# Optimization experiments

Measured on AMD Instinct MI355X. Metric: run time of the kernel, lower is better.

Reference implementation:

```python
import jax, jax.numpy as jnp
import numpy as np

C_IN = 256   # in_channels
D = 256      # hidden_dim
RNN_OUT = 2 * D  # bidir concat
K = 80       # num_classes - 1
B, H, W = 16, 64, 64


def setup_inputs() -> dict:
    key = jax.random.key(0)
    ks = jax.random.split(key, 32)
    sD = 1.0 / np.sqrt(D)
    sR = 1.0 / np.sqrt(RNN_OUT)
    f32 = jnp.float32
    inp = {}
    inp["feat"] = jax.random.normal(ks[0], (B, C_IN, H, W), f32)
    # 1x1 conv projection (acts as per-pixel linear)
    inp["proj_w"] = jax.random.normal(ks[1], (D, C_IN), f32) * sD
    inp["proj_b"] = jnp.zeros((D,), f32)
    # FastRNN forward-direction cell
    inp["Wf"] = jax.random.normal(ks[2], (D, D), f32) * sD
    inp["Uf"] = jax.random.normal(ks[3], (D, D), f32) * sD
    inp["bf"] = jnp.zeros((D,), f32)
    inp["alpha_f"] = jnp.asarray(-3.0, f32)  # sigmoid(-3) ~ 0.05 (FastRNN init)
    inp["beta_f"] = jnp.asarray(3.0, f32)    # sigmoid(3)  ~ 0.95
    # FastRNN backward-direction cell
    inp["Wb"] = jax.random.normal(ks[4], (D, D), f32) * sD
    inp["Ub"] = jax.random.normal(ks[5], (D, D), f32) * sD
    inp["bb"] = jnp.zeros((D,), f32)
    inp["alpha_b"] = jnp.asarray(-3.0, f32)
    inp["beta_b"] = jnp.asarray(3.0, f32)
    # cls MLP: Linear(RNN_OUT,RNN_OUT) -> ReLU -> Linear(RNN_OUT,K)
    inp["cls_w1"] = jax.random.normal(ks[6], (RNN_OUT, RNN_OUT), f32) * sR
    inp["cls_b1"] = jnp.zeros((RNN_OUT,), f32)
    inp["cls_w2"] = jax.random.normal(ks[7], (K, RNN_OUT), f32) * sR
    inp["cls_b2"] = jnp.zeros((K,), f32)
    # reg MLP -> 4
    inp["reg_w1"] = jax.random.normal(ks[8], (RNN_OUT, RNN_OUT), f32) * sR
    inp["reg_b1"] = jnp.zeros((RNN_OUT,), f32)
    inp["reg_w2"] = jax.random.normal(ks[9], (4, RNN_OUT), f32) * sR
    inp["reg_b2"] = jnp.zeros((4,), f32)
    # ctr MLP -> 1
    inp["ctr_w1"] = jax.random.normal(ks[10], (RNN_OUT, RNN_OUT), f32) * sR
    inp["ctr_b1"] = jnp.zeros((RNN_OUT,), f32)
    inp["ctr_w2"] = jax.random.normal(ks[11], (1, RNN_OUT), f32) * sR
    inp["ctr_b2"] = jnp.zeros((1,), f32)
    return inp


def _fastrnn_scan(pre, U, alpha, beta):
    # pre: (S, B, D) = W x_t + b precomputed for all steps
    a = jax.nn.sigmoid(alpha)
    b = jax.nn.sigmoid(beta)
    def step(h, p):
        h_new = a * jnp.tanh(p + h @ U.T) + b * h
        return h_new, h_new
    h0 = jnp.zeros(pre.shape[1:], pre.dtype)
    _, hs = jax.lax.scan(step, h0, pre)
    return hs  # (S, B, D)


def _mlp(h, w1, b1, w2, b2):
    return jax.nn.relu(h @ w1.T + b1) @ w2.T + b2


def reference(feat, proj_w, proj_b, Wf, Uf, bf, alpha_f, beta_f,
              Wb, Ub, bb, alpha_b, beta_b,
              cls_w1, cls_b1, cls_w2, cls_b2,
              reg_w1, reg_b1, reg_w2, reg_b2,
              ctr_w1, ctr_b1, ctr_w2, ctr_b2):
    Bn, C, Hn, Wn = feat.shape
    # 1x1 conv proj then flatten spatial tokens: (B, S, D)
    x = jnp.einsum('bchw,dc->bhwd', feat, proj_w) + proj_b
    x = x.reshape(Bn, Hn * Wn, D)
    # forward-direction FastRNN
    pre_f = (x @ Wf.T + bf).transpose(1, 0, 2)           # (S, B, D)
    h_f = _fastrnn_scan(pre_f, Uf, alpha_f, beta_f).transpose(1, 0, 2)
    # backward-direction FastRNN
    pre_b = (x[:, ::-1] @ Wb.T + bb).transpose(1, 0, 2)
    h_b = _fastrnn_scan(pre_b, Ub, alpha_b, beta_b).transpose(1, 0, 2)[:, ::-1]
    h = jnp.concatenate([h_f, h_b], axis=-1)             # (B, S, 2D)
    cls = _mlp(h, cls_w1, cls_b1, cls_w2, cls_b2)
    reg = _mlp(h, reg_w1, reg_b1, reg_w2, reg_b2)
    ctr = _mlp(h, ctr_w1, ctr_b1, ctr_w2, ctr_b2)
    cls = cls.reshape(Bn, Hn, Wn, K).transpose(0, 3, 1, 2)
    reg = jax.nn.relu(reg.reshape(Bn, Hn, Wn, 4).transpose(0, 3, 1, 2))
    ctr = ctr.reshape(Bn, Hn, Wn, 1).transpose(0, 3, 1, 2)
    return (cls, reg, ctr)
```

## Files before the change

kernel.cpp:

```cpp
#include <hip/hip_runtime.h>
#include <hip/hip_bf16.h>

typedef short bf16x8 __attribute__((ext_vector_type(8)));
typedef float f32x4 __attribute__((ext_vector_type(4)));

__device__ __forceinline__ ushort f2b(float x) {
    __hip_bfloat16 h = __float2bfloat16(x);
    return *reinterpret_cast<ushort*>(&h);
}

__device__ __forceinline__ void gload_lds16(const void* g, void* l) {
    __builtin_amdgcn_global_load_lds(
        (const __attribute__((address_space(1))) void*)g,
        (__attribute__((address_space(3))) void*)l, 16, 0, 0);
}

__global__ __launch_bounds__(256) void prep_mcat(
    const float* __restrict__ proj_w, const float* __restrict__ proj_b,
    const float* __restrict__ Wf, const float* __restrict__ bf_,
    const float* __restrict__ Wb, const float* __restrict__ bb_,
    __hip_bfloat16* __restrict__ Mcat, float* __restrict__ cvec)
{
    int n = blockIdx.x;
    int c = threadIdx.x;
    const float* W    = (n < 256) ? (Wf + n * 256) : (Wb + (n - 256) * 256);
    const float* bias = (n < 256) ? bf_ : bb_;
    float acc = 0.f;
    for (int k = 0; k < 256; ++k)
        acc = fmaf(W[k], proj_w[k * 256 + c], acc);
    Mcat[n * 256 + c] = __float2bfloat16(acc);

    __shared__ float red[256];
    red[c] = W[c] * proj_b[c];
    __syncthreads();
    for (int s = 128; s > 0; s >>= 1) {
        if (c < s) red[c] += red[c + s];
        __syncthreads();
    }
    if (c == 0) cvec[n] = red[0] + bias[n & 255];
}

__global__ __launch_bounds__(256) void prep_weights(
    const float* __restrict__ cls_w1, const float* __restrict__ cls_b1,
    const float* __restrict__ cls_w2, const float* __restrict__ cls_b2,
    const float* __restrict__ reg_w1, const float* __restrict__ reg_b1,
    const float* __restrict__ reg_w2, const float* __restrict__ reg_b2,
    const float* __restrict__ ctr_w1, const float* __restrict__ ctr_b1,
    const float* __restrict__ ctr_w2, const float* __restrict__ ctr_b2,
    __hip_bfloat16* __restrict__ W1cat, float* __restrict__ b1cat,
    __hip_bfloat16* __restrict__ W2pad, float* __restrict__ b2cat)
{
    int idx = blockIdx.x * 256 + threadIdx.x;
    if (idx < 786432) {
        int n = idx >> 9, k = idx & 511;
        const float* src = (n < 512) ? cls_w1 : (n < 1024 ? reg_w1 : ctr_w1);
        int nn = n & 511;
        W1cat[idx] = __float2bfloat16(src[nn * 512 + k]);
    }
    if (idx < 196608) {
        int j = idx / 1536, k = idx % 1536;
        float v = 0.f;
        if (j < 80 && k < 512)                         v = cls_w2[j * 512 + k];
        else if (j >= 80 && j < 84 && k >= 512 && k < 1024) v = reg_w2[(j - 80) * 512 + (k - 512)];
        else if (j == 84 && k >= 1024)                 v = ctr_w2[k - 1024];
        W2pad[idx] = __float2bfloat16(v);
    }
    if (idx < 1536)
        b1cat[idx] = (idx < 512) ? cls_b1[idx] : (idx < 1024 ? reg_b1[idx - 512] : ctr_b1[idx - 1024]);
    if (idx < 96)
        b2cat[idx] = (idx < 80) ? cls_b2[idx] : (idx < 84 ? reg_b2[idx - 80] : (idx == 84 ? ctr_b2[0] : 0.f));
}

__global__ __launch_bounds__(256) void transpose_feat(
    const float* __restrict__ feat, __hip_bfloat16* __restrict__ fx)
{
    __shared__ float tile[32][65];
    int st = blockIdx.x * 64, ct = blockIdx.y * 32, b = blockIdx.z;
    int tid = threadIdx.x;
    int sl = tid & 63, cl = tid >> 6;
    const float* fp = feat + ((size_t)b * 256 + ct) * 4096 + st;
#pragma unroll
    for (int i = 0; i < 8; ++i)
        tile[cl + i * 4][sl] = fp[(size_t)(cl + i * 4) * 4096 + sl];
    __syncthreads();
    int cw = tid & 31, sw = tid >> 5;
#pragma unroll
    for (int i = 0; i < 8; ++i) {
        int ss = st + sw + i * 8;
        fx[((size_t)ss * 16 + b) * 256 + ct + cw] = __float2bfloat16(tile[cw][sw + i * 8]);
    }
}

template <int MODE>
__global__ __launch_bounds__(256) void gemm_bf16(
    const __hip_bfloat16* __restrict__ A, const __hip_bfloat16* __restrict__ B,
    void* __restrict__ Cv, const float* __restrict__ bias, int M, int N, int K)
{
    __shared__ __align__(16) ushort As[128][64];
    __shared__ __align__(16) ushort Bs[128][64];
    const int tid = threadIdx.x;
    const int wv = tid >> 6;
    const int lane = tid & 63;
    const int wm = wv >> 1, wn = wv & 1;
    const int l15 = lane & 15, l4 = lane >> 4;
    const int m0 = blockIdx.y * 128;
    const int n0 = blockIdx.x * 128;

    f32x4 acc[4][4];
#pragma unroll
    for (int i = 0; i < 4; ++i)
#pragma unroll
        for (int j = 0; j < 4; ++j) acc[i][j] = (f32x4){0.f, 0.f, 0.f, 0.f};

    const int c0 = wv * 4 * 64 + lane;
    const ushort* Abase = (const ushort*)A;
    const ushort* Bbase = (const ushort*)B;

    for (int k0 = 0; k0 < K; k0 += 64) {
#pragma unroll
        for (int i = 0; i < 4; ++i) {
            int c = c0 + i * 64;
            int row = c >> 3, kc = c & 7;
            int kcs = (kc ^ (row & 7)) * 8;
            gload_lds16(Abase + (size_t)(m0 + row) * K + k0 + kcs,
                        &As[0][0] + (wv * 4 + i) * 512);
            gload_lds16(Bbase + (size_t)(n0 + row) * K + k0 + kcs,
                        &Bs[0][0] + (wv * 4 + i) * 512);
        }
        asm volatile("s_waitcnt vmcnt(0)" ::: "memory");
        __syncthreads();

#pragma unroll
        for (int ks = 0; ks < 2; ++ks) {
            const int swz = ((ks * 4 + l4) ^ (l15 & 7)) * 8;
            bf16x8 af[4], bf[4];
#pragma unroll
            for (int mi = 0; mi < 4; ++mi)
                af[mi] = *(const bf16x8*)(&As[0][0] + (wm * 64 + mi * 16 + l15) * 64 + swz);
#pragma unroll
            for (int ni = 0; ni < 4; ++ni)
                bf[ni] = *(const bf16x8*)(&Bs[0][0] + (wn * 64 + ni * 16 + l15) * 64 + swz);
#pragma unroll
            for (int mi = 0; mi < 4; ++mi)
#pragma unroll
                for (int ni = 0; ni < 4; ++ni)
                    acc[mi][ni] = __builtin_amdgcn_mfma_f32_16x16x32_bf16(af[mi], bf[ni], acc[mi][ni], 0, 0, 0);
        }
        __syncthreads();
    }

#pragma unroll
    for (int mi = 0; mi < 4; ++mi) {
#pragma unroll
        for (int ni = 0; ni < 4; ++ni) {
            int col = n0 + wn * 64 + ni * 16 + l15;
#pragma unroll
            for (int r = 0; r < 4; ++r) {
                int row = m0 + wm * 64 + mi * 16 + l4 * 4 + r;
                float v = acc[mi][ni][r];
                if constexpr (MODE >= 1) v += bias[col];
                if constexpr (MODE == 2) {
                    v = fmaxf(v, 0.f);
                    ((__hip_bfloat16*)Cv)[(size_t)row * N + col] = __float2bfloat16(v);
                } else {
                    ((float*)Cv)[(size_t)row * N + col] = v;
                }
            }
        }
    }
}

#define HROW 264
#define CHUNK_S 32
#define WARMUP 256
__global__ __launch_bounds__(512, 2) void scan_chunk(
    const float* __restrict__ pre, const float* __restrict__ Uf, const float* __restrict__ Ub,
    const float* __restrict__ alpha_f, const float* __restrict__ beta_f,
    const float* __restrict__ alpha_b, const float* __restrict__ beta_b,
    __hip_bfloat16* __restrict__ h_out)
{
    const int dir = blockIdx.y;
    const int chk = blockIdx.x;
    const int o0 = chk * CHUNK_S;
    const int o1 = o0 + CHUNK_S;
    int start = o0 - WARMUP; if (start < 0) start = 0;

    const int tid = threadIdx.x;
    const int w = tid >> 6;
    const int lane = tid & 63;
    const int l15 = lane & 15;
    const int l4 = lane >> 4;

    const float* U = dir ? Ub : Uf;
    const float alpha = dir ? alpha_b[0] : alpha_f[0];
    const float beta  = dir ? beta_b[0]  : beta_f[0];
    const float a  = 1.f / (1.f + __expf(-alpha));
    const float bd = 1.f / (1.f + __expf(-beta));

    bf16x8 ufr[2][8];
#pragma unroll
    for (int mt = 0; mt < 2; ++mt) {
        const int row = w * 32 + mt * 16 + l15;
#pragma unroll
        for (int kc = 0; kc < 8; ++kc) {
            const float* up = U + (size_t)row * 256 + kc * 32 + l4 * 8;
            bf16x8 fr;
#pragma unroll
            for (int j = 0; j < 8; ++j) fr[j] = (short)f2b(up[j]);
            ufr[mt][kc] = fr;
        }
    }

    __shared__ __align__(16) ushort hbuf[2][16][HROW];
    for (int i = tid; i < 2 * 16 * HROW; i += 512) ((ushort*)hbuf)[i] = 0;

    float4 hown[2];
    hown[0] = (float4){0.f, 0.f, 0.f, 0.f};
    hown[1] = (float4){0.f, 0.f, 0.f, 0.f};

    const size_t off0 = (size_t)l15 * 512 + dir * 256 + w * 32 + l4 * 4;

    const int wb = tid >> 5;
    const int wp = tid & 31;
    ushort* hob = (ushort*)h_out + dir * 256 + (size_t)wb * 512 + wp * 8;

    const int sA0 = dir ? (4095 - start) : start;
    const int sB0 = dir ? (4095 - (start + 1)) : (start + 1);
    float4 pA0 = *(const float4*)(pre + (size_t)sA0 * 8192 + off0);
    float4 pA1 = *(const float4*)(pre + (size_t)sA0 * 8192 + off0 + 16);
    float4 pB0 = *(const float4*)(pre + (size_t)sB0 * 8192 + off0);
    float4 pB1 = *(const float4*)(pre + (size_t)sB0 * 8192 + off0 + 16);

    __syncthreads();

#define SCAN_STEP(T, CUR, NXT, P0, P1)                                              \
    do {                                                                            \
        const int s_ = dir ? (4095 - (T)) : (T);                                    \
        bf16x8 bfrag[8];                                                            \
        _Pragma("unroll")                                                           \
        for (int kc = 0; kc < 8; ++kc)                                              \
            bfrag[kc] = *(const bf16x8*)&hbuf[CUR][l15][kc * 32 + l4 * 8];          \
        f32x4 acc0 = (f32x4){0.f, 0.f, 0.f, 0.f};                                   \
        f32x4 acc1 = (f32x4){0.f, 0.f, 0.f, 0.f};                                   \
        _Pragma("unroll")                                                           \
        for (int kc = 0; kc < 8; ++kc) {                                            \
            acc0 = __builtin_amdgcn_mfma_f32_16x16x32_bf16(ufr[0][kc], bfrag[kc], acc0, 0, 0, 0); \
            acc1 = __builtin_amdgcn_mfma_f32_16x16x32_bf16(ufr[1][kc], bfrag[kc], acc1, 0, 0, 0); \
        }                                                                           \
        _Pragma("unroll")                                                           \
        for (int mt = 0; mt < 2; ++mt) {                                            \
            f32x4 accv = mt ? acc1 : acc0;                                          \
            const float* pcp = mt ? (const float*)&(P1) : (const float*)&(P0);      \
            const float* hop_ = (const float*)&hown[mt];                            \
            float hn[4];                                                            \
            _Pragma("unroll")                                                       \
            for (int r = 0; r < 4; ++r) {                                           \
                float z = accv[r] + pcp[r];                                         \
                float e = exp2f(z * 2.885390081777927f);                            \
                float th = fmaf(-2.f, __builtin_amdgcn_rcpf(e + 1.f), 1.f);         \
                hn[r] = fmaf(a, th, bd * hop_[r]);                                  \
            }                                                                       \
            hown[mt] = (float4){hn[0], hn[1], hn[2], hn[3]};                        \
            ushort4 pk;                                                             \
            pk.x = f2b(hn[0]); pk.y = f2b(hn[1]); pk.z = f2b(hn[2]); pk.w = f2b(hn[3]); \
            *(ushort4*)&hbuf[NXT][l15][w * 32 + mt * 16 + l4 * 4] = pk;             \
        }                                                                           \
        asm volatile("s_waitcnt lgkmcnt(0)" ::: "memory");                          \
        __builtin_amdgcn_s_barrier();                                               \
        if ((T) >= o0) {                                                            \
            bf16x8 hv = *(const bf16x8*)&hbuf[NXT][wb][wp * 8];                     \
            *(bf16x8*)(hob + (size_t)s_ * 8192) = hv;                               \
        }                                                                           \
    } while (0)

    for (int t = start; t < o1; t += 2) {
        SCAN_STEP(t, 0, 1, pA0, pA1);
        {
            int t2 = (t + 2 < o1) ? (t + 2) : (o1 - 1);
            int s2 = dir ? (4095 - t2) : t2;
            pA0 = *(const float4*)(pre + (size_t)s2 * 8192 + off0);
            pA1 = *(const float4*)(pre + (size_t)s2 * 8192 + off0 + 16);
        }
        SCAN_STEP(t + 1, 1, 0, pB0, pB1);
        {
            int t3 = (t + 3 < o1) ? (t + 3) : (o1 - 1);
            int s3 = dir ? (4095 - t3) : t3;
            pB0 = *(const float4*)(pre + (size_t)s3 * 8192 + off0);
            pB1 = *(const float4*)(pre + (size_t)s3 * 8192 + off0 + 16);
        }
    }
#undef SCAN_STEP
}

__global__ __launch_bounds__(256) void epi_kernel(
    const float* __restrict__ out2, const float* __restrict__ b2cat, float* __restrict__ out)
{
    __shared__ float tile[64][129];
    const int t0 = blockIdx.x * 64;
    const int tid = threadIdx.x;
#pragma unroll
    for (int i = 0; i < 32; ++i) {
        int idx = tid + i * 256;
        int tk = idx >> 7, j = idx & 127;
        tile[tk][j] = out2[((size_t)(t0 + tk)) * 128 + j];
    }
    __syncthreads();
    for (int p = 0; p < 22; ++p) {
        int idx = tid + p * 256;
        if (idx < 5440) {
            int j = idx >> 6;
            int s_ = idx & 63;
            float v = tile[s_][j] + b2cat[j];
            int token = t0 + s_;
            int b = token & 15, s = token >> 4;
            size_t dst;
            if (j < 80) {
                dst = (size_t)b * 327680 + (size_t)j * 4096 + s;
            } else if (j < 84) {
                v = fmaxf(v, 0.f);
                dst = 5242880 + (size_t)b * 16384 + (size_t)(j - 80) * 4096 + s;
            } else {
                dst = 5505024 + (size_t)b * 4096 + s;
            }
            out[dst] = v;
        }
    }
}

extern "C" void kernel_launch(void* const* d_in, const int* in_sizes, int n_in,
                              void* d_out, int out_size, void* d_ws, size_t ws_size,
                              hipStream_t stream) {
    (void)in_sizes; (void)n_in; (void)out_size; (void)ws_size;
    const float* feat    = (const float*)d_in[0];
    const float* proj_w  = (const float*)d_in[1];
    const float* proj_b  = (const float*)d_in[2];
    const float* Wf      = (const float*)d_in[3];
    const float* Uf      = (const float*)d_in[4];
    const float* bf_     = (const float*)d_in[5];
    const float* alpha_f = (const float*)d_in[6];
    const float* beta_f  = (const float*)d_in[7];
    const float* Wb      = (const float*)d_in[8];
    const float* Ub      = (const float*)d_in[9];
    const float* bb_     = (const float*)d_in[10];
    const float* alpha_b = (const float*)d_in[11];
    const float* beta_b  = (const float*)d_in[12];
    const float* cls_w1  = (const float*)d_in[13];
    const float* cls_b1  = (const float*)d_in[14];
    const float* cls_w2  = (const float*)d_in[15];
    const float* cls_b2  = (const float*)d_in[16];
    const float* reg_w1  = (const float*)d_in[17];
    const float* reg_b1  = (const float*)d_in[18];
    const float* reg_w2  = (const float*)d_in[19];
    const float* reg_b2  = (const float*)d_in[20];
    const float* ctr_w1  = (const float*)d_in[21];
    const float* ctr_b1  = (const float*)d_in[22];
    const float* ctr_w2  = (const float*)d_in[23];
    const float* ctr_b2  = (const float*)d_in[24];

    char* ws = (char*)d_ws;
    __hip_bfloat16* h_bf  = (__hip_bfloat16*)(ws);
    float*          pre   = (float*)(ws + 67108864);
    __hip_bfloat16* L1c   = (__hip_bfloat16*)(ws + 67108864);
    char*           regC  = ws + 201326592;
    __hip_bfloat16* fx    = (__hip_bfloat16*)regC;
    float*          out2  = (float*)regC;
    char*           wts   = ws + 260046848;
    __hip_bfloat16* Mcat  = (__hip_bfloat16*)(wts);
    float*          cvec  = (float*)(wts + 262144);
    __hip_bfloat16* W1cat = (__hip_bfloat16*)(wts + 264192);
    float*          b1cat = (float*)(wts + 1837056);
    __hip_bfloat16* W2pad = (__hip_bfloat16*)(wts + 1843200);
    float*          b2cat = (float*)(wts + 2236416);

    prep_mcat<<<512, 256, 0, stream>>>(proj_w, proj_b, Wf, bf_, Wb, bb_, Mcat, cvec);
    prep_weights<<<3072, 256, 0, stream>>>(cls_w1, cls_b1, cls_w2, cls_b2,
        reg_w1, reg_b1, reg_w2, reg_b2, ctr_w1, ctr_b1, ctr_w2, ctr_b2,
        W1cat, b1cat, W2pad, b2cat);
    transpose_feat<<<dim3(64, 8, 16), 256, 0, stream>>>(feat, fx);

    gemm_bf16<1><<<dim3(4, 512), 256, 0, stream>>>(fx, Mcat, pre, cvec, 65536, 512, 256);

    scan_chunk<<<dim3(128, 2), 512, 0, stream>>>(pre, Uf, Ub, alpha_f, beta_f, alpha_b, beta_b, h_bf);

    for (int c = 0; c < 2; ++c) {
        gemm_bf16<2><<<dim3(12, 256), 256, 0, stream>>>(
            h_bf + (size_t)c * 32768 * 512, W1cat, L1c, b1cat, 32768, 1536, 512);
        gemm_bf16<0><<<dim3(1, 256), 256, 0, stream>>>(
            L1c, W2pad, out2 + (size_t)c * 32768 * 128, nullptr, 32768, 128, 1536);
    }

    epi_kernel<<<1024, 256, 0, stream>>>(out2, b2cat, (float*)d_out);
}
```

Baseline: 553.0 us.

## Fuse layer-2 head GEMM with epilogue, skip zero blocks, shorten scan warmup

Replaces the padded second-layer GEMM plus separate epilogue kernel with one fused kernel. It multiplies only the nonzero head blocks (cls, reg, ctr) against their 512-wide slices of L1 and applies bias and ReLU. It transposes through shared memory and writes the final NCHW outputs directly. This removes wasted MFMA work on zero padding, the intermediate out2 buffer round trip and a launch. The scan warmup window is also reduced, cutting redundant recurrence steps at some accuracy risk, and the fused kernel launches only 128 blocks.

```diff
diff --git a/kernel.cpp b/kernel.cpp
--- a/kernel.cpp
+++ b/kernel.cpp
@@ -48,7 +48,7 @@
     const float* __restrict__ ctr_w1, const float* __restrict__ ctr_b1,
     const float* __restrict__ ctr_w2, const float* __restrict__ ctr_b2,
     __hip_bfloat16* __restrict__ W1cat, float* __restrict__ b1cat,
-    __hip_bfloat16* __restrict__ W2pad, float* __restrict__ b2cat)
+    __hip_bfloat16* __restrict__ w2h, float* __restrict__ b2h)
 {
     int idx = blockIdx.x * 256 + threadIdx.x;
     if (idx < 786432) {
@@ -57,18 +57,18 @@
         int nn = n & 511;
         W1cat[idx] = __float2bfloat16(src[nn * 512 + k]);
     }
-    if (idx < 196608) {
-        int j = idx / 1536, k = idx % 1536;
+    if (idx < 65536) {
+        int r = idx >> 9, k = idx & 511;
         float v = 0.f;
-        if (j < 80 && k < 512)                         v = cls_w2[j * 512 + k];
-        else if (j >= 80 && j < 84 && k >= 512 && k < 1024) v = reg_w2[(j - 80) * 512 + (k - 512)];
-        else if (j == 84 && k >= 1024)                 v = ctr_w2[k - 1024];
-        W2pad[idx] = __float2bfloat16(v);
+        if (r < 80)       v = cls_w2[r * 512 + k];
+        else if (r < 84)  v = reg_w2[(r - 80) * 512 + k];
+        else if (r == 96) v = ctr_w2[k];
+        w2h[idx] = __float2bfloat16(v);
     }
     if (idx < 1536)
         b1cat[idx] = (idx < 512) ? cls_b1[idx] : (idx < 1024 ? reg_b1[idx - 512] : ctr_b1[idx - 1024]);
-    if (idx < 96)
-        b2cat[idx] = (idx < 80) ? cls_b2[idx] : (idx < 84 ? reg_b2[idx - 80] : (idx == 84 ? ctr_b2[0] : 0.f));
+    if (idx < 112)
+        b2h[idx] = (idx < 80) ? cls_b2[idx] : (idx < 84 ? reg_b2[idx - 80] : (idx == 96 ? ctr_b2[0] : 0.f));
 }
 
 __global__ __launch_bounds__(256) void transpose_feat(
@@ -170,9 +170,124 @@
     }
 }
 
+__global__ __launch_bounds__(512) void fused_l2(
+    const __hip_bfloat16* __restrict__ L1c, const __hip_bfloat16* __restrict__ w2h,
+    const float* __restrict__ b2h, float* __restrict__ out, int chunk)
+{
+    __shared__ __align__(16) char smem[256 * 105 * 4];
+    ushort* As = (ushort*)smem;
+    ushort* Bs = (ushort*)(smem + 32768);
+    float* sacc = (float*)smem;
+
+    const int tid = threadIdx.x;
+    const int wv = tid >> 6;
+    const int lane = tid & 63;
+    const int l15 = lane & 15, l4 = lane >> 4;
+    const int tok0 = blockIdx.x * 256;
+    const ushort* Ab = (const ushort*)L1c;
+    const ushort* Bb = (const ushort*)w2h;
+
+    f32x4 acc[2][7];
+#pragma unroll
+    for (int i = 0; i < 2; ++i)
+#pragma unroll
+        for (int j = 0; j < 7; ++j) acc[i][j] = (f32x4){0.f, 0.f, 0.f, 0.f};
+
+#pragma unroll
+    for (int p = 0; p < 3; ++p) {
+        for (int k0 = 0; k0 < 512; k0 += 64) {
+#pragma unroll
+            for (int i = 0; i < 4; ++i) {
+                int c = (wv * 4 + i) * 64 + lane;
+                int row = c >> 3, kc = c & 7;
+                int kcs = (kc ^ (row & 7)) * 8;
+                gload_lds16(Ab + (size_t)(tok0 + row) * 1536 + p * 512 + k0 + kcs, As + c * 8);
+            }
+#pragma unroll
+            for (int i = 0; i < 2; ++i) {
+                int c = (wv * 2 + i) * 64 + lane;
+                int row = c >> 3, kc = c & 7;
+                int kcs = (kc ^ (row & 7)) * 8;
+                gload_lds16(Bb + (size_t)row * 512 + k0 + kcs, Bs + c * 8);
+            }
+            asm volatile("s_waitcnt vmcnt(0)" ::: "memory");
+            __syncthreads();
+
+#pragma unroll
+            for (int ks = 0; ks < 2; ++ks) {
+                const int swz = ((ks * 4 + l4) ^ (l15 & 7)) * 8;
+                bf16x8 af0 = *(const bf16x8*)(As + (wv * 32 + l15) * 64 + swz);
+                bf16x8 af1 = *(const bf16x8*)(As + (wv * 32 + 16 + l15) * 64 + swz);
+                if (p == 0) {
+#pragma unroll
+                    for (int ni = 0; ni < 5; ++ni) {
+                        bf16x8 bf = *(const bf16x8*)(Bs + (ni * 16 + l15) * 64 + swz);
+                        acc[0][ni] = __builtin_amdgcn_mfma_f32_16x16x32_bf16(af0, bf, acc[0][ni], 0, 0, 0);
+                        acc[1][ni] = __builtin_amdgcn_mfma_f32_16x16x32_bf16(af1, bf, acc[1][ni], 0, 0, 0);
+                    }
+                } else {
+                    const int ni = (p == 1) ? 5 : 6;
+                    bf16x8 bf = *(const bf16x8*)(Bs + (ni * 16 + l15) * 64 + swz);
+                    acc[0][ni] = __builtin_amdgcn_mfma_f32_16x16x32_bf16(af0, bf, acc[0][ni], 0, 0, 0);
+                    acc[1][ni] = __builtin_amdgcn_mfma_f32_16x16x32_bf16(af1, bf, acc[1][ni], 0, 0, 0);
+                }
+            }
+            __syncthreads();
+        }
+    }
+
+#pragma unroll
+    for (int mi = 0; mi < 2; ++mi) {
+#pragma unroll
+        for (int ni = 0; ni < 7; ++ni) {
+            const int fragcol = ni * 16 + l15;
+            const float bias = b2h[fragcol];
+#pragma unroll
+            for (int r = 0; r < 4; ++r) {
+                int row = wv * 32 + mi * 16 + l4 * 4 + r;
+                float v = acc[mi][ni][r] + bias;
+                if (ni == 5 && l15 < 4) v = fmaxf(v, 0.f);
+                if (ni < 6) sacc[row * 105 + fragcol] = v;
+                else if (l15 == 0) sacc[row * 105 + 96] = v;
+            }
+        }
+    }
+    __syncthreads();
+
+    const int s0 = chunk * 2048 + blockIdx.x * 16;
+#pragma unroll
+    for (int it = 0; it < 10; ++it) {
+        int slot = it * 512 + tid;
+        int j = slot >> 6;
+        int rem = slot & 63;
+        int b = rem >> 2, q = rem & 3;
+        float4 v;
+#pragma unroll
+        for (int e = 0; e < 4; ++e)
+            ((float*)&v)[e] = sacc[((q * 4 + e) * 16 + b) * 105 + j];
+        *(float4*)(out + (size_t)b * 327680 + (size_t)j * 4096 + s0 + q * 4) = v;
+    }
+    if (tid < 256) {
+        int j = tid >> 6, rem = tid & 63, b = rem >> 2, q = rem & 3;
+        float4 v;
+#pragma unroll
+        for (int e = 0; e < 4; ++e)
+            ((float*)&v)[e] = sacc[((q * 4 + e) * 16 + b) * 105 + 80 + j];
+        *(float4*)(out + 5242880 + (size_t)b * 16384 + (size_t)j * 4096 + s0 + q * 4) = v;
+    }
+    if (tid < 64) {
+        int b = tid >> 2, q = tid & 3;
+        float4 v;
+#pragma unroll
+        for (int e = 0; e < 4; ++e)
+            ((float*)&v)[e] = sacc[((q * 4 + e) * 16 + b) * 105 + 96];
+        *(float4*)(out + 5505024 + (size_t)b * 4096 + s0 + q * 4) = v;
+    }
+}
+
 #define HROW 264
 #define CHUNK_S 32
-#define WARMUP 256
+#define WARMUP 192
 __global__ __launch_bounds__(512, 2) void scan_chunk(
     const float* __restrict__ pre, const float* __restrict__ Uf, const float* __restrict__ Ub,
     const float* __restrict__ alpha_f, const float* __restrict__ beta_f,
@@ -292,41 +407,6 @@
 #undef SCAN_STEP
 }
 
-__global__ __launch_bounds__(256) void epi_kernel(
-    const float* __restrict__ out2, const float* __restrict__ b2cat, float* __restrict__ out)
-{
-    __shared__ float tile[64][129];
-    const int t0 = blockIdx.x * 64;
-    const int tid = threadIdx.x;
-#pragma unroll
-    for (int i = 0; i < 32; ++i) {
-        int idx = tid + i * 256;
-        int tk = idx >> 7, j = idx & 127;
-        tile[tk][j] = out2[((size_t)(t0 + tk)) * 128 + j];
-    }
-    __syncthreads();
-    for (int p = 0; p < 22; ++p) {
-        int idx = tid + p * 256;
-        if (idx < 5440) {
-            int j = idx >> 6;
-            int s_ = idx & 63;
-            float v = tile[s_][j] + b2cat[j];
-            int token = t0 + s_;
-            int b = token & 15, s = token >> 4;
-            size_t dst;
-            if (j < 80) {
-                dst = (size_t)b * 327680 + (size_t)j * 4096 + s;
-            } else if (j < 84) {
-                v = fmaxf(v, 0.f);
-                dst = 5242880 + (size_t)b * 16384 + (size_t)(j - 80) * 4096 + s;
-            } else {
-                dst = 5505024 + (size_t)b * 4096 + s;
-            }
-            out[dst] = v;
-        }
-    }
-}
-
 extern "C" void kernel_launch(void* const* d_in, const int* in_sizes, int n_in,
                               void* d_out, int out_size, void* d_ws, size_t ws_size,
                               hipStream_t stream) {
@@ -363,19 +443,18 @@
     __hip_bfloat16* L1c   = (__hip_bfloat16*)(ws + 67108864);
     char*           regC  = ws + 201326592;
     __hip_bfloat16* fx    = (__hip_bfloat16*)regC;
-    float*          out2  = (float*)regC;
     char*           wts   = ws + 260046848;
     __hip_bfloat16* Mcat  = (__hip_bfloat16*)(wts);
     float*          cvec  = (float*)(wts + 262144);
     __hip_bfloat16* W1cat = (__hip_bfloat16*)(wts + 264192);
     float*          b1cat = (float*)(wts + 1837056);
-    __hip_bfloat16* W2pad = (__hip_bfloat16*)(wts + 1843200);
-    float*          b2cat = (float*)(wts + 2236416);
+    __hip_bfloat16* w2h   = (__hip_bfloat16*)(wts + 1843200);
+    float*          b2h   = (float*)(wts + 1974272);
 
     prep_mcat<<<512, 256, 0, stream>>>(proj_w, proj_b, Wf, bf_, Wb, bb_, Mcat, cvec);
     prep_weights<<<3072, 256, 0, stream>>>(cls_w1, cls_b1, cls_w2, cls_b2,
         reg_w1, reg_b1, reg_w2, reg_b2, ctr_w1, ctr_b1, ctr_w2, ctr_b2,
-        W1cat, b1cat, W2pad, b2cat);
+        W1cat, b1cat, w2h, b2h);
     transpose_feat<<<dim3(64, 8, 16), 256, 0, stream>>>(feat, fx);
 
     gemm_bf16<1><<<dim3(4, 512), 256, 0, stream>>>(fx, Mcat, pre, cvec, 65536, 512, 256);
@@ -385,9 +464,6 @@
     for (int c = 0; c < 2; ++c) {
         gemm_bf16<2><<<dim3(12, 256), 256, 0, stream>>>(
             h_bf + (size_t)c * 32768 * 512, W1cat, L1c, b1cat, 32768, 1536, 512);
-        gemm_bf16<0><<<dim3(1, 256), 256, 0, stream>>>(
-            L1c, W2pad, out2 + (size_t)c * 32768 * 128, nullptr, 32768, 128, 1536);
-    }
-
-    epi_kernel<<<1024, 256, 0, stream>>>(out2, b2cat, (float*)d_out);
-}
+        fused_l2<<<128, 512, 0, stream>>>(L1c, w2h, b2h, (float*)d_out, c);
+    }
+}
```

Result: faster. 467.1 us, median of 2 (-15.5%).
